# Kernel tuning notes

Hardware: AMD Instinct MI355X
Metric: run time of the kernel (lower is better)

## Reference

```python
import jax, jax.numpy as jnp
from jax import lax
import numpy as np

T, D, H, E, K = 4096, 1024, 2048, 8, 2

def setup_inputs() -> dict:
    key = jax.random.key(0)
    ks = jax.random.split(key, 5)
    x = jax.random.normal(ks[0], (T, D), dtype=jnp.float32)
    weights = jax.random.uniform(ks[1], (T, K), dtype=jnp.float32)
    indices = jax.random.randint(ks[2], (T, K), 0, E, dtype=jnp.int64)
    # GatedMLP params (bias=False): fc1 weight [2H, D], fc2 weight [D, H], stacked over experts
    W1 = jax.random.normal(ks[3], (E, 2 * H, D), dtype=jnp.float32) * 0.02
    W2 = jax.random.normal(ks[4], (E, D, H), dtype=jnp.float32) * 0.02
    return {"x": x, "weights": weights, "indices": indices, "W1": W1, "W2": W2}

def reference(x, weights, indices, W1, W2):
    # Combine per-token routing weights into a per-(token, expert) weight matrix.
    # Tokens not routed to expert e get weight 0, so the dense per-expert GatedMLP
    # weighted-sum is mathematically identical to the gather->MLP->scatter-add loop.
    onehot = jax.nn.one_hot(indices, E, dtype=weights.dtype)        # [T, K, E]
    w_te = jnp.einsum('tke,tk->et', onehot, weights)                # [E, T]

    def body(y, carry):
        W1e, W2e, we = carry                                        # [2H,D], [D,H], [T]
        h = x @ W1e.T                                               # [T, 2H]
        u, gate = jnp.split(h, 2, axis=-1)                          # [T, H] each
        out = (u * jax.nn.silu(gate)) @ W2e.T                       # [T, D]
        return y + out * we[:, None], None

    y, _ = lax.scan(body, jnp.zeros_like(x), (W1, W2, w_te))
    return y
```

## Files before the change

kernel.cpp:

```cpp
#include <hip/hip_runtime.h>
#include <stdint.h>

#define T_TOK 4096
#define D_DIM 1024
#define H_DIM 2048
#define E_EXP 8
#define K_TOP 2
#define NTK   (T_TOK * K_TOP)
#define MT1 256
#define MAXT1 48

typedef short bf16x8 __attribute__((ext_vector_type(8)));
typedef float f32x4  __attribute__((ext_vector_type(4)));

#define MINI(a, b) ((a) < (b) ? (a) : (b))
#define MFMA_BF16 __builtin_amdgcn_mfma_f32_16x16x32_bf16

__device__ __forceinline__ unsigned short f2bf(float f) {
  unsigned u = __float_as_uint(f);
  u += 0x7fffu + ((u >> 16) & 1u);
  return (unsigned short)(u >> 16);
}

#define GLDS16(gp, lp)                                                        \
  __builtin_amdgcn_global_load_lds(                                           \
      (const __attribute__((address_space(1))) void*)(gp),                    \
      (__attribute__((address_space(3))) void*)(lp), 16, 0, 0)


#define NX8   (T_TOK * D_DIM / 8)
#define NW18  (E_EXP * 2 * H_DIM * D_DIM / 8)
#define NW28  (E_EXP * D_DIM * H_DIM / 8)
#define PRE_CVT_BLKS ((NX8 + NW18) / 256)
#define PRE_BLKS (PRE_CVT_BLKS + 32)

__global__ __launch_bounds__(256) void k_pre(const float* __restrict__ x,
                                             const float* __restrict__ W1,
                                             const int* __restrict__ idx,
                                             unsigned short* __restrict__ xb,
                                             unsigned short* __restrict__ W1b,
                                             int* __restrict__ meta) {
  int bid = blockIdx.x;
  int tid = threadIdx.x;
  if (bid >= PRE_CVT_BLKS) {
    __shared__ int h[E_EXP];
    if (tid < E_EXP) h[tid] = 0;
    __syncthreads();
    int i = (bid - PRE_CVT_BLKS) * 256 + tid;
    atomicAdd(&h[idx[i] & (E_EXP - 1)], 1);
    __syncthreads();
    if (tid < E_EXP) atomicAdd(&meta[tid], h[tid]);
    return;
  }
  long gid = (long)bid * 256 + tid;
  const float* src;
  unsigned short* dst;
  long i;
  if (gid < NX8) { src = x; dst = xb; i = gid; }
  else           { src = W1; dst = W1b; i = gid - NX8; }
  float4 a = ((const float4*)src)[2 * i];
  float4 b = ((const float4*)src)[2 * i + 1];
  uint4 o;
  o.x = f2bf(a.x) | ((unsigned)f2bf(a.y) << 16);
  o.y = f2bf(a.z) | ((unsigned)f2bf(a.w) << 16);
  o.z = f2bf(b.x) | ((unsigned)f2bf(b.y) << 16);
  o.w = f2bf(b.z) | ((unsigned)f2bf(b.w) << 16);
  ((uint4*)dst)[i] = o;
}

__global__ __launch_bounds__(64) void k_route_plan(int* __restrict__ meta) {
  if (threadIdx.x) return;
  int off = 0, nt = 0;
  for (int e = 0; e < E_EXP; ++e) {
    int c = meta[e];
    meta[8 + e]  = off;
    meta[16 + e] = off;
    for (int r = 0; r < c; r += MT1) {
      meta[32 + nt]  = e;
      meta[80 + nt]  = off + r;
      meta[128 + nt] = MINI(MT1, c - r);
      ++nt;
    }
    off += c;
  }
  meta[24] = nt;
}

__global__ __launch_bounds__(256) void k_route_scatter(const int* __restrict__ idx,
                                                       const float* __restrict__ w,
                                                       int* __restrict__ meta,
                                                       int* __restrict__ rows,
                                                       float* __restrict__ wv) {
  __shared__ int h[E_EXP], base[E_EXP];
  int tid = threadIdx.x;
  if (tid < E_EXP) h[tid] = 0;
  __syncthreads();
  int i = blockIdx.x * 256 + tid;
  int e = idx[i] & (E_EXP - 1);
  int r = atomicAdd(&h[e], 1);
  __syncthreads();
  if (tid < E_EXP) base[tid] = atomicAdd(&meta[16 + tid], h[tid]);
  __syncthreads();
  int p = base[e] + r;
  rows[p] = i >> 1;
  wv[p]   = w[i];
}

#define G1_TILES (MAXT1 * 32)
#define CVW2_BLK 1024
#define ZOUT_BLK 64
#define G1_GRID  (G1_TILES + CVW2_BLK + ZOUT_BLK)

__global__ __launch_bounds__(256, 2) void k_gemm1(
    const unsigned short* __restrict__ xb,
    const unsigned short* __restrict__ W1b,
    const int* __restrict__ meta,
    const int* __restrict__ rows,
    const float* __restrict__ wv,
    unsigned short* __restrict__ act,
    const float* __restrict__ W2,
    unsigned short* __restrict__ W2b,
    float* __restrict__ out) {
  int bid = blockIdx.x;
  int tid = threadIdx.x;

  if (bid >= G1_TILES) {
    int xb2 = bid - G1_TILES;
    if (xb2 < CVW2_BLK) {
      long g0 = (long)xb2 * 256 + tid;
      for (long i = g0; i < NW28; i += (long)CVW2_BLK * 256) {
        float4 a = ((const float4*)W2)[2 * i];
        float4 b = ((const float4*)W2)[2 * i + 1];
        uint4 o;
        o.x = f2bf(a.x) | ((unsigned)f2bf(a.y) << 16);
        o.y = f2bf(a.z) | ((unsigned)f2bf(a.w) << 16);
        o.z = f2bf(b.x) | ((unsigned)f2bf(b.y) << 16);
        o.w = f2bf(b.z) | ((unsigned)f2bf(b.w) << 16);
        ((uint4*)W2b)[i] = o;
      }
    } else {
      int zb = xb2 - CVW2_BLK;
      long g0 = (long)zb * 256 + tid;
      uint4 z = {0u, 0u, 0u, 0u};
      for (long i = g0; i < (long)(T_TOK * D_DIM / 4); i += (long)ZOUT_BLK * 256)
        ((uint4*)out)[i] = z;
    }
    return;
  }

  int nt = meta[24];
  int tb = bid % MAXT1;
  int y  = bid / MAXT1;
  if (tb >= nt) return;
  int e     = meta[32 + tb];
  int r0    = meta[80 + tb];
  int valid = meta[128 + tb];
  int n0    = y << 6;

  __shared__ unsigned short lA[256 * 64];
  __shared__ unsigned short lB1[64 * 64];
  __shared__ unsigned short lB2[64 * 64];
  __shared__ float sw[256];

  int wave = tid >> 6, lane = tid & 63;

  sw[tid] = wv[r0 + MINI(tid, valid - 1)];

  const unsigned short* w1e = W1b + (size_t)e * (4096 * 1024);

  const unsigned short *pA[8], *pB1[2], *pB2[2];
#pragma unroll
  for (int it = 0; it < 8; ++it) {
    int c = it * 256 + tid;
    int r = c >> 3, cc = c & 7;
    int g = cc ^ (r & 7);
    int tok = rows[r0 + MINI(r, valid - 1)];
    pA[it] = xb + (size_t)tok * 1024 + g * 8;
  }
#pragma unroll
  for (int it = 0; it < 2; ++it) {
    int c = it * 256 + tid;
    int r = c >> 3, cc = c & 7;
    int g = cc ^ (r & 7);
    pB1[it] = w1e + (size_t)(n0 + r) * 1024 + g * 8;
    pB2[it] = w1e + (size_t)(2048 + n0 + r) * 1024 + g * 8;
  }

  f32x4 zero = {0.f, 0.f, 0.f, 0.f};
  f32x4 au[4][4], ag[4][4];
#pragma unroll
  for (int i = 0; i < 4; ++i)
#pragma unroll
    for (int j = 0; j < 4; ++j) { au[i][j] = zero; ag[i][j] = zero; }

  int mb = wave * 64;
  int fr = lane & 15, q = lane >> 4;

  for (int k0 = 0; k0 < 1024; k0 += 64) {
    __syncthreads();
#pragma unroll
    for (int it = 0; it < 8; ++it)
      GLDS16(pA[it] + k0, &lA[(it * 256 + wave * 64) * 8]);
#pragma unroll
    for (int it = 0; it < 2; ++it) {
      int lb = (it * 256 + wave * 64) * 8;
      GLDS16(pB1[it] + k0, &lB1[lb]);
      GLDS16(pB2[it] + k0, &lB2[lb]);
    }
    __syncthreads();
#pragma unroll
    for (int kk = 0; kk < 2; ++kk) {
      int co = (((kk << 2) + q) ^ (fr & 7)) * 8 + fr * 64;
      bf16x8 a[4];
#pragma unroll
      for (int i = 0; i < 4; ++i)
        a[i] = *(const bf16x8*)&lA[(mb + i * 16) * 64 + co];
#pragma unroll
      for (int j = 0; j < 4; ++j) {
        bf16x8 bu = *(const bf16x8*)&lB1[(j * 16) * 64 + co];
        bf16x8 bg = *(const bf16x8*)&lB2[(j * 16) * 64 + co];
#pragma unroll
        for (int i = 0; i < 4; ++i) {
          au[i][j] = MFMA_BF16(a[i], bu, au[i][j], 0, 0, 0);
          ag[i][j] = MFMA_BF16(a[i], bg, ag[i][j], 0, 0, 0);
        }
      }
    }
  }

#pragma unroll
  for (int i = 0; i < 4; ++i) {
#pragma unroll
    for (int reg = 0; reg < 4; ++reg) {
      int lm = mb + i * 16 + q * 4 + reg;
      if (lm < valid) {
        float wrow = sw[lm];
        size_t orow = (size_t)(r0 + lm) * 2048;
#pragma unroll
        for (int j = 0; j < 4; ++j) {
          float u = au[i][j][reg];
          float g = ag[i][j][reg];
          float s = g / (1.f + __expf(-g));
          act[orow + (n0 + j * 16 + fr)] = f2bf(u * s * wrow);
        }
      }
    }
  }
}

__global__ __launch_bounds__(256, 2) void k_gemm2(
    const unsigned short* __restrict__ act,
    const unsigned short* __restrict__ W2b,
    const int* __restrict__ meta,
    const int* __restrict__ rows,
    float* __restrict__ out) {
  int nt = meta[24];
  int tb = blockIdx.x;
  if (tb >= nt) return;
  int e     = meta[32 + tb];
  int r0    = meta[80 + tb];
  int valid = meta[128 + tb];
  int n0    = blockIdx.y * 128;

  __shared__ unsigned short lA[256 * 64];
  __shared__ unsigned short lB[128 * 64];
  __shared__ int st[256];

  int tid = threadIdx.x;
  int wave = tid >> 6, lane = tid & 63;
  st[tid] = rows[r0 + MINI(tid, valid - 1)];

  const unsigned short* w2e = W2b + (size_t)e * (1024 * 2048);

  const unsigned short *pA[8], *pB[4];
#pragma unroll
  for (int it = 0; it < 8; ++it) {
    int c = it * 256 + tid;
    int r = c >> 3, cc = c & 7;
    int g = cc ^ (r & 7);
    pA[it] = act + (size_t)(r0 + MINI(r, valid - 1)) * 2048 + g * 8;
  }
#pragma unroll
  for (int it = 0; it < 4; ++it) {
    int c = it * 256 + tid;
    int r = c >> 3, cc = c & 7;
    int g = cc ^ (r & 7);
    pB[it] = w2e + (size_t)(n0 + r) * 2048 + g * 8;
  }

  f32x4 zero = {0.f, 0.f, 0.f, 0.f};
  f32x4 acc[4][8];
#pragma unroll
  for (int i = 0; i < 4; ++i)
#pragma unroll
    for (int j = 0; j < 8; ++j) acc[i][j] = zero;

  int mb = wave * 64;
  int fr = lane & 15, q = lane >> 4;

  for (int k0 = 0; k0 < 2048; k0 += 64) {
    __syncthreads();
#pragma unroll
    for (int it = 0; it < 8; ++it)
      GLDS16(pA[it] + k0, &lA[(it * 256 + wave * 64) * 8]);
#pragma unroll
    for (int it = 0; it < 4; ++it)
      GLDS16(pB[it] + k0, &lB[(it * 256 + wave * 64) * 8]);
    __syncthreads();
#pragma unroll
    for (int kk = 0; kk < 2; ++kk) {
      int co = (((kk << 2) + q) ^ (fr & 7)) * 8 + fr * 64;
      bf16x8 a[4];
#pragma unroll
      for (int i = 0; i < 4; ++i)
        a[i] = *(const bf16x8*)&lA[(mb + i * 16) * 64 + co];
#pragma unroll
      for (int j = 0; j < 8; ++j) {
        bf16x8 b = *(const bf16x8*)&lB[(j * 16) * 64 + co];
#pragma unroll
        for (int i = 0; i < 4; ++i)
          acc[i][j] = MFMA_BF16(a[i], b, acc[i][j], 0, 0, 0);
      }
    }
  }

#pragma unroll
  for (int i = 0; i < 4; ++i) {
#pragma unroll
    for (int reg = 0; reg < 4; ++reg) {
      int lm = mb + i * 16 + q * 4 + reg;
      if (lm < valid) {
        int tok = st[lm];
        float* op = out + (size_t)tok * 1024;
#pragma unroll
        for (int j = 0; j < 8; ++j)
          atomicAdd(&op[n0 + j * 16 + fr], acc[i][j][reg]);
      }
    }
  }
}

extern "C" void kernel_launch(void* const* d_in, const int* in_sizes, int n_in,
                              void* d_out, int out_size, void* d_ws, size_t ws_size,
                              hipStream_t stream) {
  const float* x  = (const float*)d_in[0];
  const float* w  = (const float*)d_in[1];
  const int*  idx = (const int*)d_in[2];
  const float* W1 = (const float*)d_in[3];
  const float* W2 = (const float*)d_in[4];
  float* out = (float*)d_out;

  char* ws = (char*)d_ws;
  unsigned short* W1b = (unsigned short*)(ws);
  unsigned short* W2b = (unsigned short*)(ws + 67108864);
  unsigned short* xb  = (unsigned short*)(ws + 100663296);
  unsigned short* act = (unsigned short*)(ws + 109051904);
  int*   rows = (int*)(ws + 142606336);
  float* wv   = (float*)(ws + 142639104);
  int*   meta = (int*)(ws + 142671872);

  hipMemsetAsync(meta, 0, 1024, stream);

  k_pre<<<PRE_BLKS, 256, 0, stream>>>(x, W1, idx, xb, W1b, meta);
  k_route_plan<<<1, 64, 0, stream>>>(meta);
  k_route_scatter<<<32, 256, 0, stream>>>(idx, w, meta, rows, wv);

  k_gemm1<<<G1_GRID, 256, 0, stream>>>(xb, W1b, meta, rows, wv, act,
                                       W2, W2b, out);

  dim3 g2(MAXT1, D_DIM / 128);
  k_gemm2<<<g2, 256, 0, stream>>>(act, W2b, meta, rows, out);
}
```

Measured before the change: 423.0 us.

## Replace atomic scatter-add with per-slot stores and a combine kernel; drop route-plan launch

GEMM2 now writes each routed slot's output row to a per-slot fp32 buffer with plain stores instead of doing fp32 atomicAdd into the token output. A new combine kernel sums the two slot rows per token, which also removes the need to zero the output inside gemm1. The single-thread route-plan kernel is removed, and tiles are found on the fly by a small prefix scan over the expert counts in each block. Row and slot indices become 16-bit. The cost is an extra 32 MB write and read of slot outputs, which reuse the W1 bf16 buffer region, plus one more launch.

```diff
diff --git a/kernel.cpp b/kernel.cpp
--- a/kernel.cpp
+++ b/kernel.cpp
@@ -27,6 +27,23 @@
       (const __attribute__((address_space(1))) void*)(gp),                    \
       (__attribute__((address_space(3))) void*)(lp), 16, 0, 0)
 
+
+__device__ __forceinline__ bool tile_lookup(const int* __restrict__ meta,
+                                            int tb, int& e, int& r0, int& valid) {
+  int off = 0, acc = 0;
+  e = -1; r0 = 0; valid = 0;
+#pragma unroll
+  for (int ee = 0; ee < E_EXP; ++ee) {
+    int c = meta[ee];
+    int ntl = (c + MT1 - 1) >> 8;
+    int loc = tb - acc;
+    if (loc >= 0 && loc < ntl) {
+      e = ee; r0 = off + (loc << 8); valid = MINI(MT1, c - (loc << 8));
+    }
+    acc += ntl; off += c;
+  }
+  return e >= 0;
+}
 
 #define NX8   (T_TOK * D_DIM / 8)
 #define NW18  (E_EXP * 2 * H_DIM * D_DIM / 8)
@@ -68,28 +85,11 @@
   ((uint4*)dst)[i] = o;
 }
 
-__global__ __launch_bounds__(64) void k_route_plan(int* __restrict__ meta) {
-  if (threadIdx.x) return;
-  int off = 0, nt = 0;
-  for (int e = 0; e < E_EXP; ++e) {
-    int c = meta[e];
-    meta[8 + e]  = off;
-    meta[16 + e] = off;
-    for (int r = 0; r < c; r += MT1) {
-      meta[32 + nt]  = e;
-      meta[80 + nt]  = off + r;
-      meta[128 + nt] = MINI(MT1, c - r);
-      ++nt;
-    }
-    off += c;
-  }
-  meta[24] = nt;
-}
-
 __global__ __launch_bounds__(256) void k_route_scatter(const int* __restrict__ idx,
                                                        const float* __restrict__ w,
                                                        int* __restrict__ meta,
-                                                       int* __restrict__ rows,
+                                                       unsigned short* __restrict__ rows,
+                                                       unsigned short* __restrict__ slotpos,
                                                        float* __restrict__ wv) {
   __shared__ int h[E_EXP], base[E_EXP];
   int tid = threadIdx.x;
@@ -99,63 +99,56 @@
   int e = idx[i] & (E_EXP - 1);
   int r = atomicAdd(&h[e], 1);
   __syncthreads();
-  if (tid < E_EXP) base[tid] = atomicAdd(&meta[16 + tid], h[tid]);
+  if (tid < E_EXP) {
+    int off = 0;
+#pragma unroll
+    for (int ee = 0; ee < E_EXP; ++ee)
+      if (ee < tid) off += meta[ee];
+    base[tid] = off + atomicAdd(&meta[16 + tid], h[tid]);
+  }
   __syncthreads();
   int p = base[e] + r;
-  rows[p] = i >> 1;
-  wv[p]   = w[i];
+  rows[p]    = (unsigned short)(i >> 1);
+  slotpos[i] = (unsigned short)p;
+  wv[p]      = w[i];
 }
 
 #define G1_TILES (MAXT1 * 32)
 #define CVW2_BLK 1024
-#define ZOUT_BLK 64
-#define G1_GRID  (G1_TILES + CVW2_BLK + ZOUT_BLK)
+#define G1_GRID  (G1_TILES + CVW2_BLK)
 
 __global__ __launch_bounds__(256, 2) void k_gemm1(
     const unsigned short* __restrict__ xb,
     const unsigned short* __restrict__ W1b,
     const int* __restrict__ meta,
-    const int* __restrict__ rows,
+    const unsigned short* __restrict__ rows,
     const float* __restrict__ wv,
     unsigned short* __restrict__ act,
     const float* __restrict__ W2,
-    unsigned short* __restrict__ W2b,
-    float* __restrict__ out) {
+    unsigned short* __restrict__ W2b) {
   int bid = blockIdx.x;
   int tid = threadIdx.x;
 
   if (bid >= G1_TILES) {
-    int xb2 = bid - G1_TILES;
-    if (xb2 < CVW2_BLK) {
-      long g0 = (long)xb2 * 256 + tid;
-      for (long i = g0; i < NW28; i += (long)CVW2_BLK * 256) {
-        float4 a = ((const float4*)W2)[2 * i];
-        float4 b = ((const float4*)W2)[2 * i + 1];
-        uint4 o;
-        o.x = f2bf(a.x) | ((unsigned)f2bf(a.y) << 16);
-        o.y = f2bf(a.z) | ((unsigned)f2bf(a.w) << 16);
-        o.z = f2bf(b.x) | ((unsigned)f2bf(b.y) << 16);
-        o.w = f2bf(b.z) | ((unsigned)f2bf(b.w) << 16);
-        ((uint4*)W2b)[i] = o;
-      }
-    } else {
-      int zb = xb2 - CVW2_BLK;
-      long g0 = (long)zb * 256 + tid;
-      uint4 z = {0u, 0u, 0u, 0u};
-      for (long i = g0; i < (long)(T_TOK * D_DIM / 4); i += (long)ZOUT_BLK * 256)
-        ((uint4*)out)[i] = z;
+    long g0 = (long)(bid - G1_TILES) * 256 + tid;
+    for (long i = g0; i < NW28; i += (long)CVW2_BLK * 256) {
+      float4 a = ((const float4*)W2)[2 * i];
+      float4 b = ((const float4*)W2)[2 * i + 1];
+      uint4 o;
+      o.x = f2bf(a.x) | ((unsigned)f2bf(a.y) << 16);
+      o.y = f2bf(a.z) | ((unsigned)f2bf(a.w) << 16);
+      o.z = f2bf(b.x) | ((unsigned)f2bf(b.y) << 16);
+      o.w = f2bf(b.z) | ((unsigned)f2bf(b.w) << 16);
+      ((uint4*)W2b)[i] = o;
     }
     return;
   }
 
-  int nt = meta[24];
   int tb = bid % MAXT1;
   int y  = bid / MAXT1;
-  if (tb >= nt) return;
-  int e     = meta[32 + tb];
-  int r0    = meta[80 + tb];
-  int valid = meta[128 + tb];
-  int n0    = y << 6;
+  int e, r0, valid;
+  if (!tile_lookup(meta, tb, e, r0, valid)) return;
+  int n0 = y << 6;
 
   __shared__ unsigned short lA[256 * 64];
   __shared__ unsigned short lB1[64 * 64];
@@ -252,23 +245,17 @@
     const unsigned short* __restrict__ act,
     const unsigned short* __restrict__ W2b,
     const int* __restrict__ meta,
-    const int* __restrict__ rows,
-    float* __restrict__ out) {
-  int nt = meta[24];
+    float* __restrict__ y) {
   int tb = blockIdx.x;
-  if (tb >= nt) return;
-  int e     = meta[32 + tb];
-  int r0    = meta[80 + tb];
-  int valid = meta[128 + tb];
-  int n0    = blockIdx.y * 128;
+  int e, r0, valid;
+  if (!tile_lookup(meta, tb, e, r0, valid)) return;
+  int n0 = blockIdx.y * 128;
 
   __shared__ unsigned short lA[256 * 64];
   __shared__ unsigned short lB[128 * 64];
-  __shared__ int st[256];
 
   int tid = threadIdx.x;
   int wave = tid >> 6, lane = tid & 63;
-  st[tid] = rows[r0 + MINI(tid, valid - 1)];
 
   const unsigned short* w2e = W2b + (size_t)e * (1024 * 2048);
 
@@ -330,14 +317,28 @@
     for (int reg = 0; reg < 4; ++reg) {
       int lm = mb + i * 16 + q * 4 + reg;
       if (lm < valid) {
-        int tok = st[lm];
-        float* op = out + (size_t)tok * 1024;
+        float* yp = y + (size_t)(r0 + lm) * 1024 + n0;
 #pragma unroll
         for (int j = 0; j < 8; ++j)
-          atomicAdd(&op[n0 + j * 16 + fr], acc[i][j][reg]);
+          yp[j * 16 + fr] = acc[i][j][reg];
       }
     }
   }
+}
+
+__global__ __launch_bounds__(256) void k_combine(
+    const float* __restrict__ y,
+    const unsigned short* __restrict__ slotpos,
+    float* __restrict__ out) {
+  int t = blockIdx.x;
+  int s0 = slotpos[2 * t], s1 = slotpos[2 * t + 1];
+  const float4* a = (const float4*)(y + (size_t)s0 * 1024);
+  const float4* b = (const float4*)(y + (size_t)s1 * 1024);
+  float4* o = (float4*)(out + (size_t)t * 1024);
+  int d = threadIdx.x;
+  float4 va = a[d], vb = b[d];
+  float4 vo = {va.x + vb.x, va.y + vb.y, va.z + vb.z, va.w + vb.w};
+  o[d] = vo;
 }
 
 extern "C" void kernel_launch(void* const* d_in, const int* in_sizes, int n_in,
@@ -352,22 +353,24 @@
 
   char* ws = (char*)d_ws;
   unsigned short* W1b = (unsigned short*)(ws);
+  float*          yslot = (float*)(ws);
   unsigned short* W2b = (unsigned short*)(ws + 67108864);
   unsigned short* xb  = (unsigned short*)(ws + 100663296);
   unsigned short* act = (unsigned short*)(ws + 109051904);
-  int*   rows = (int*)(ws + 142606336);
+  unsigned short* rows    = (unsigned short*)(ws + 142606336);
+  unsigned short* slotpos = (unsigned short*)(ws + 142622720);
   float* wv   = (float*)(ws + 142639104);
   int*   meta = (int*)(ws + 142671872);
 
   hipMemsetAsync(meta, 0, 1024, stream);
 
   k_pre<<<PRE_BLKS, 256, 0, stream>>>(x, W1, idx, xb, W1b, meta);
-  k_route_plan<<<1, 64, 0, stream>>>(meta);
-  k_route_scatter<<<32, 256, 0, stream>>>(idx, w, meta, rows, wv);
-
-  k_gemm1<<<G1_GRID, 256, 0, stream>>>(xb, W1b, meta, rows, wv, act,
-                                       W2, W2b, out);
+  k_route_scatter<<<32, 256, 0, stream>>>(idx, w, meta, rows, slotpos, wv);
+
+  k_gemm1<<<G1_GRID, 256, 0, stream>>>(xb, W1b, meta, rows, wv, act, W2, W2b);
 
   dim3 g2(MAXT1, D_DIM / 128);
-  k_gemm2<<<g2, 256, 0, stream>>>(act, W2b, meta, rows, out);
-}
+  k_gemm2<<<g2, 256, 0, stream>>>(act, W2b, meta, yslot);
+
+  k_combine<<<T_TOK, 256, 0, stream>>>(yslot, slotpos, out);
+}
```

Result: faster. 407.9 us (-3.6%).
